# Kernel tuning notes

Measured on AMD Instinct MI355X. Metric: run time of the kernel, lower is better.

The kernel has to match this reference:

```python
import jax, jax.numpy as jnp
import numpy as np

BETA = 0.95
THR = 1.0
SLOPE = 25.0


@jax.custom_vjp
def spike(x):
    # Heaviside spike with fast-sigmoid surrogate gradient (snntorch fast_sigmoid, slope=25)
    return (x > 0).astype(x.dtype)

def _spike_fwd(x):
    return spike(x), x

def _spike_bwd(x, g):
    sg = 1.0 / (SLOPE * jnp.abs(x) + 1.0) ** 2
    return (g * sg,)

spike.defvjp(_spike_fwd, _spike_bwd)


def setup_inputs() -> dict:
    key = jax.random.key(0)
    k_x, k_w1, k_b1, k_w2, k_b2 = jax.random.split(key, 5)
    T, B, D_IN, H, OUT = 30, 4096, 784, 128, 10
    x = jax.random.uniform(k_x, (T, B, D_IN), dtype=jnp.float32)
    # PyTorch nn.Linear default init: U(-1/sqrt(fan_in), 1/sqrt(fan_in))
    lim1 = 1.0 / np.sqrt(D_IN)
    lim2 = 1.0 / np.sqrt(H)
    W1 = jax.random.uniform(k_w1, (H, D_IN), jnp.float32, -lim1, lim1)
    b1 = jax.random.uniform(k_b1, (H,), jnp.float32, -lim1, lim1)
    W2 = jax.random.uniform(k_w2, (OUT, H), jnp.float32, -lim2, lim2)
    b2 = jax.random.uniform(k_b2, (OUT,), jnp.float32, -lim2, lim2)
    return {"x": x, "W1": W1, "b1": b1, "W2": W2, "b2": b2}


def reference(x, W1, b1, W2, b2):
    T, B, _ = x.shape
    H, OUT = W1.shape[0], W2.shape[0]

    def step(carry, xt):
        mem1, mem2 = carry
        # layer 1: linear + leaky integrate-and-fire (reset by subtraction)
        cur1 = xt @ W1.T + b1  # [B, H]
        reset1 = jax.lax.stop_gradient((mem1 - THR > 0).astype(xt.dtype))
        mem1 = BETA * mem1 + cur1 - reset1 * THR
        spk1 = spike(mem1 - THR)
        # layer 2
        cur2 = spk1 @ W2.T + b2  # [B, OUT]
        reset2 = jax.lax.stop_gradient((mem2 - THR > 0).astype(xt.dtype))
        mem2 = BETA * mem2 + cur2 - reset2 * THR
        spk2 = spike(mem2 - THR)
        return (mem1, mem2), (spk2, mem2)

    init = (jnp.zeros((B, H), x.dtype), jnp.zeros((B, OUT), x.dtype))
    _, (spk2_rec, mem2_rec) = jax.lax.scan(step, init, x)
    return spk2_rec, mem2_rec  # each [T, B, OUT]
```

## Files before the change

### kernel.cpp

```cpp
#include <hip/hip_runtime.h>
#include <stdint.h>

#define THR  1.0f
#define BETA 0.95f
#define SX   4096.0f
#define SW   512.0f
#define SINV (1.0f / (4096.0f * 512.0f))
#define W1N  (128 * 784)

typedef __attribute__((ext_vector_type(8)))  _Float16 f16x8;
typedef __attribute__((ext_vector_type(16))) float    f32x16;
typedef __attribute__((ext_vector_type(4)))  float    fvec4;

__device__ __forceinline__ void gll16(const float* g, float* l){
  __builtin_amdgcn_global_load_lds((const __attribute__((address_space(1))) void*)g,
                                   (__attribute__((address_space(3))) void*)l, 16, 0, 0);
}

__global__ void split_w1(const float* __restrict__ W1, _Float16* __restrict__ wB){
  int i = blockIdx.x * 256 + threadIdx.x;
  if (i < W1N) {
    int h = i / 784, k = i % 784;
    float v = W1[i] * SW;
    _Float16 hi = (_Float16)v;
    _Float16 lo = (_Float16)(v - (float)hi);
    int ks = k >> 4, kg = (k >> 3) & 1, j = k & 7, nf = h >> 5, r = h & 31;
    int base = ((ks * 4 + nf) * 2) * 512 + (kg * 32 + r) * 8 + j;
    wB[base]       = hi;
    wB[base + 512] = lo;
  }
}

__launch_bounds__(256, 2)
__global__ void gemm1(const float* __restrict__ x,
                      const float* __restrict__ wBf,
                      const float* __restrict__ b1,
                      float* __restrict__ cur1,
                      long row0){
  __shared__ float lds[16384];
  const int lane = threadIdx.x & 63;
  const int w    = threadIdx.x >> 6;
  const long blk_row0 = row0 + (long)blockIdx.x * 128;
  const int r  = lane & 31;
  const int kg = lane >> 5;

  const float* xA  = x + (blk_row0 + w * 32 + r) * 784 + kg * 8;
  const float* wBs = wBf + w * 512 + lane * 4;

  #define STAGE(bb, s) {                                                     \
    gll16(xA  + (s) * 16,       &lds[(bb) * 4096 + (w * 2 + 0) * 256]);      \
    gll16(xA  + (s) * 16 + 4,   &lds[(bb) * 4096 + (w * 2 + 1) * 256]);      \
    gll16(wBs + (s) * 2048,     &lds[(bb) * 4096 + 2048 + (w * 2 + 0) * 256]); \
    gll16(wBs + (s) * 2048 + 256, &lds[(bb) * 4096 + 2048 + (w * 2 + 1) * 256]); }

  #define COMPUTE(bb) {                                                      \
    f16x8 b[8];                                                              \
    _Pragma("unroll") for (int f = 0; f < 8; ++f)                            \
      b[f] = *(const f16x8*)&lds[(bb) * 4096 + 2048 + f * 256 + lane * 4];   \
    fvec4 a0 = *(const fvec4*)&lds[(bb) * 4096 + (w * 2 + 0) * 256 + lane * 4]; \
    fvec4 a1 = *(const fvec4*)&lds[(bb) * 4096 + (w * 2 + 1) * 256 + lane * 4]; \
    f16x8 ah, al;                                                            \
    _Pragma("unroll") for (int j = 0; j < 8; ++j) {                          \
      float v = ((j < 4) ? a0[j] : a1[j - 4]) * SX;                          \
      _Float16 hh = (_Float16)v;                                             \
      ah[j] = hh; al[j] = (_Float16)(v - (float)hh);                         \
    }                                                                        \
    _Pragma("unroll") for (int nf = 0; nf < 4; ++nf) {                       \
      acc[nf] = __builtin_amdgcn_mfma_f32_32x32x16_f16(ah, b[nf * 2],     acc[nf], 0, 0, 0); \
      acc[nf] = __builtin_amdgcn_mfma_f32_32x32x16_f16(ah, b[nf * 2 + 1], acc[nf], 0, 0, 0); \
      acc[nf] = __builtin_amdgcn_mfma_f32_32x32x16_f16(al, b[nf * 2],     acc[nf], 0, 0, 0); \
    } }

  #define FENCE_A() { __builtin_amdgcn_sched_barrier(0);                     \
    asm volatile("s_waitcnt lgkmcnt(0)" ::: "memory");                       \
    __builtin_amdgcn_s_barrier();                                            \
    asm volatile("" ::: "memory"); }
  #define FENCE_B(vm) {                                                      \
    asm volatile("s_waitcnt vmcnt(" #vm ")" ::: "memory");                   \
    __builtin_amdgcn_s_barrier();                                            \
    asm volatile("" ::: "memory");                                           \
    __builtin_amdgcn_sched_barrier(0); }

  f32x16 acc[4] = {};

  STAGE(0, 0); STAGE(1, 1); STAGE(2, 2); STAGE(3, 3);
  FENCE_B(12);
  COMPUTE(0);

  for (int q = 0; q < 11; ++q) {
    const int s = 4 * q + 1;
    FENCE_A(); STAGE(0, s + 3); FENCE_B(12); COMPUTE(1);
    FENCE_A(); STAGE(1, s + 4); FENCE_B(12); COMPUTE(2);
    FENCE_A(); STAGE(2, s + 5); FENCE_B(12); COMPUTE(3);
    FENCE_A(); STAGE(3, s + 6); FENCE_B(12); COMPUTE(0);
  }

  FENCE_A(); STAGE(0, 48); FENCE_B(12); COMPUTE(1);
  FENCE_A();               FENCE_B(8);  COMPUTE(2);
  FENCE_A();               FENCE_B(4);  COMPUTE(3);
  FENCE_A();               FENCE_B(0);  COMPUTE(0);

  float b1v[4];
  #pragma unroll
  for (int nf = 0; nf < 4; ++nf) b1v[nf] = b1[nf * 32 + r];
  long m0 = (long)blockIdx.x * 128 + w * 32;
  #pragma unroll
  for (int nf = 0; nf < 4; ++nf)
    #pragma unroll
    for (int reg = 0; reg < 16; ++reg) {
      int rr = (reg & 3) + 8 * (reg >> 2) + 4 * kg;
      cur1[(m0 + rr) * 128 + nf * 32 + r] = acc[nf][reg] * SINV + b1v[nf];
    }
  #undef STAGE
  #undef COMPUTE
  #undef FENCE_A
  #undef FENCE_B
}

__launch_bounds__(256)
__global__ void lif(const float* __restrict__ cur1,
                    const float* __restrict__ W2,
                    const float* __restrict__ b2,
                    float* __restrict__ out,
                    float* __restrict__ state1,
                    float* __restrict__ state2,
                    int t0, int tn){
  const int lane = threadIdx.x & 63;
  const int b = blockIdx.x * 4 + (threadIdx.x >> 6);
  const int o = lane & 15;
  const int c = lane >> 4;

  float wv[32];
  #pragma unroll
  for (int j = 0; j < 32; ++j) wv[j] = 0.f;
  if (o < 10) {
    #pragma unroll
    for (int j = 0; j < 32; ++j) wv[j] = W2[o * 128 + c * 32 + j];
  }
  float b2v = (lane < 10) ? b2[lane] : 0.f;

  float mem1a, mem1b, mem2;
  if (t0 == 0) { mem1a = 0.f; mem1b = 0.f; mem2 = 0.f; }
  else {
    mem1a = state1[b * 128 + lane];
    mem1b = state1[b * 128 + 64 + lane];
    mem2  = (lane < 10) ? state2[b * 10 + lane] : 0.f;
  }

  for (int t = t0; t < tn; ++t) {
    long base = ((long)(t - t0) * 4096 + b) * 128;
    float c1a = cur1[base + lane];
    float c1b = cur1[base + 64 + lane];
    float r1a = (mem1a > THR) ? THR : 0.f;
    float r1b = (mem1b > THR) ? THR : 0.f;
    mem1a = BETA * mem1a + c1a - r1a;
    mem1b = BETA * mem1b + c1b - r1b;

    uint64_t mA = __ballot(mem1a > THR);
    uint64_t mB = __ballot(mem1b > THR);
    uint64_t m64 = (c & 2) ? mB : mA;
    uint32_t bits = (uint32_t)(m64 >> ((c & 1) << 5));

    float s = 0.f;
    #pragma unroll
    for (int j = 0; j < 32; ++j)
      s = fmaf((float)((bits >> j) & 1u), wv[j], s);
    s += __shfl_xor(s, 16);
    s += __shfl_xor(s, 32);

    if (lane < 10) {
      float cur2 = s + b2v;
      float r2 = (mem2 > THR) ? THR : 0.f;
      mem2 = BETA * mem2 + cur2 - r2;
      float s2 = (mem2 > THR) ? 1.f : 0.f;
      long ob = (long)t * 40960 + (long)b * 10 + lane;
      out[ob] = s2;
      out[1228800 + ob] = mem2;
    }
  }

  if (tn < 30) {
    state1[b * 128 + lane] = mem1a;
    state1[b * 128 + 64 + lane] = mem1b;
    if (lane < 10) state2[b * 10 + lane] = mem2;
  }
}

extern "C" void kernel_launch(void* const* d_in, const int* in_sizes, int n_in,
                              void* d_out, int out_size, void* d_ws, size_t ws_size,
                              hipStream_t stream) {
  const float* x  = (const float*)d_in[0];
  const float* W1 = (const float*)d_in[1];
  const float* b1 = (const float*)d_in[2];
  const float* W2 = (const float*)d_in[3];
  const float* b2 = (const float*)d_in[4];
  float* out = (float*)d_out;

  const int T = 30, B = 4096;

  char* ws = (char*)d_ws;
  _Float16* wB = (_Float16*)ws;
  size_t off = (size_t)49 * 8 * 512 * sizeof(_Float16);
  off = (off + 255) & ~(size_t)255;
  float* state1 = (float*)(ws + off); off += (size_t)B * 128 * 4;
  float* state2 = (float*)(ws + off); off += (size_t)B * 10 * 4;
  off = (off + 255) & ~(size_t)255;
  float* cur1 = (float*)(ws + off);

  size_t per_t = (size_t)B * 128 * 4;
  size_t avail = (ws_size > off) ? (ws_size - off) : 0;
  int CH = (int)(avail / per_t);
  if (CH > T) CH = T;
  if (CH < 1) CH = 1;

  split_w1<<<(W1N + 255) / 256, 256, 0, stream>>>(W1, wB);

  for (int t0 = 0; t0 < T; t0 += CH) {
    int tn = (t0 + CH < T) ? (t0 + CH) : T;
    int mrows = (tn - t0) * B;
    gemm1<<<mrows / 128, 256, 0, stream>>>(x, (const float*)wB, b1, cur1, (long)t0 * B);
    lif<<<B / 4, 256, 0, stream>>>(cur1, W2, b2, out, state1, state2, t0, tn);
  }
}
```

Measured before the change: 172.4 us.

## Deepen gemm1 LDS ring to five stages and drop the per-step read fence

The gemm1 shared-memory staging ring grows from four buffers to five (LDS grows from 64KB to 80KB per block). The main loop is restructured so that each step issues the next async global-to-LDS load, waits on vmcnt, and then computes. A buffer is now only overwritten two steps after it was read, so the separate lgkmcnt wait plus extra barrier (FENCE_A) can be removed, halving barriers per k-step. The cost is more LDS per block: at 2 blocks per CU this needs 160KB, which may limit occupancy if the CU's LDS budget is tighter than that.

```diff
diff --git a/kernel.cpp b/kernel.cpp
--- a/kernel.cpp
+++ b/kernel.cpp
@@ -37,7 +37,7 @@
                       const float* __restrict__ b1,
                       float* __restrict__ cur1,
                       long row0){
-  __shared__ float lds[16384];
+  __shared__ float lds[20480];
   const int lane = threadIdx.x & 63;
   const int w    = threadIdx.x >> 6;
   const long blk_row0 = row0 + (long)blockIdx.x * 128;
@@ -48,12 +48,12 @@
   const float* wBs = wBf + w * 512 + lane * 4;
 
   #define STAGE(bb, s) {                                                     \
-    gll16(xA  + (s) * 16,       &lds[(bb) * 4096 + (w * 2 + 0) * 256]);      \
-    gll16(xA  + (s) * 16 + 4,   &lds[(bb) * 4096 + (w * 2 + 1) * 256]);      \
-    gll16(wBs + (s) * 2048,     &lds[(bb) * 4096 + 2048 + (w * 2 + 0) * 256]); \
+    gll16(xA  + (s) * 16,         &lds[(bb) * 4096 + (w * 2 + 0) * 256]);    \
+    gll16(xA  + (s) * 16 + 4,     &lds[(bb) * 4096 + (w * 2 + 1) * 256]);    \
+    gll16(wBs + (s) * 2048,       &lds[(bb) * 4096 + 2048 + (w * 2 + 0) * 256]); \
     gll16(wBs + (s) * 2048 + 256, &lds[(bb) * 4096 + 2048 + (w * 2 + 1) * 256]); }
 
-  #define COMPUTE(bb) {                                                      \
+  #define CPH(bb) {                                                          \
     f16x8 b[8];                                                              \
     _Pragma("unroll") for (int f = 0; f < 8; ++f)                            \
       b[f] = *(const f16x8*)&lds[(bb) * 4096 + 2048 + f * 256 + lane * 4];   \
@@ -71,11 +71,7 @@
       acc[nf] = __builtin_amdgcn_mfma_f32_32x32x16_f16(al, b[nf * 2],     acc[nf], 0, 0, 0); \
     } }
 
-  #define FENCE_A() { __builtin_amdgcn_sched_barrier(0);                     \
-    asm volatile("s_waitcnt lgkmcnt(0)" ::: "memory");                       \
-    __builtin_amdgcn_s_barrier();                                            \
-    asm volatile("" ::: "memory"); }
-  #define FENCE_B(vm) {                                                      \
+  #define VMB(vm) {                                                          \
     asm volatile("s_waitcnt vmcnt(" #vm ")" ::: "memory");                   \
     __builtin_amdgcn_s_barrier();                                            \
     asm volatile("" ::: "memory");                                           \
@@ -83,22 +79,20 @@
 
   f32x16 acc[4] = {};
 
-  STAGE(0, 0); STAGE(1, 1); STAGE(2, 2); STAGE(3, 3);
-  FENCE_B(12);
-  COMPUTE(0);
-
-  for (int q = 0; q < 11; ++q) {
-    const int s = 4 * q + 1;
-    FENCE_A(); STAGE(0, s + 3); FENCE_B(12); COMPUTE(1);
-    FENCE_A(); STAGE(1, s + 4); FENCE_B(12); COMPUTE(2);
-    FENCE_A(); STAGE(2, s + 5); FENCE_B(12); COMPUTE(3);
-    FENCE_A(); STAGE(3, s + 6); FENCE_B(12); COMPUTE(0);
-  }
-
-  FENCE_A(); STAGE(0, 48); FENCE_B(12); COMPUTE(1);
-  FENCE_A();               FENCE_B(8);  COMPUTE(2);
-  FENCE_A();               FENCE_B(4);  COMPUTE(3);
-  FENCE_A();               FENCE_B(0);  COMPUTE(0);
+  STAGE(0, 0); STAGE(1, 1); STAGE(2, 2);
+
+  for (int g = 0; g < 9; ++g) {
+    const int s5 = 5 * g;
+    STAGE(3, s5 + 3); VMB(12); CPH(0);
+    STAGE(4, s5 + 4); VMB(12); CPH(1);
+    STAGE(0, s5 + 5); VMB(12); CPH(2);
+    STAGE(1, s5 + 6); VMB(12); CPH(3);
+    STAGE(2, s5 + 7); VMB(12); CPH(4);
+  }
+  STAGE(3, 48); VMB(12); CPH(0);
+  VMB(8);  CPH(1);
+  VMB(4);  CPH(2);
+  VMB(0);  CPH(3);
 
   float b1v[4];
   #pragma unroll
@@ -112,9 +106,8 @@
       cur1[(m0 + rr) * 128 + nf * 32 + r] = acc[nf][reg] * SINV + b1v[nf];
     }
   #undef STAGE
-  #undef COMPUTE
-  #undef FENCE_A
-  #undef FENCE_B
+  #undef CPH
+  #undef VMB
 }
 
 __launch_bounds__(256)
```

Measured after the change: 171.1 us. No clear change (-0.8%).
